# Performance work log

Hardware: AMD Instinct MI355X
Metric: run time of the kernel (lower is better)

Reference implementation:

```python
import jax, jax.numpy as jnp
import numpy as np

BLOCKS = (1, 2, 3, 4)      # (block_size, offset=0) from max_block_size=4
BLOCK_MULT = 12            # lcm(1,2,3,4)
DS = 4                     # downsample_factor
MAX_BS = 4                 # max block size (also pos_conv kernel size)
DIM = 512
VOCAB = 256


def _masked_mean(t, m, axis):
    # t: [..., L, D], m: [..., L] bool -> mean over axis with mask, 0 where empty
    mf = m[..., None].astype(t.dtype)
    num = jnp.sum(t * mf, axis=axis)
    tot = jnp.sum(mf, axis=axis)
    mean = num / jnp.clip(tot, 1.0)
    return jnp.where(tot == 0.0, jnp.zeros_like(mean), mean)


def setup_inputs() -> dict:
    key = jax.random.key(0)
    ks = jax.random.split(key, 8)
    B, S = 8, 2048
    return {
        "x": jax.random.randint(ks[0], (B, S), 0, VOCAB),
        "mask": jnp.ones((B, S), dtype=bool),
        "emb": jax.random.normal(ks[1], (VOCAB, DIM), jnp.float32) * 0.02,
        "dw_w": jax.random.normal(ks[2], (MAX_BS, 1, DIM), jnp.float32) * 0.1,   # depthwise kernel (W, I=1, O=DIM)
        "dw_b": jnp.zeros((DIM,), jnp.float32),
        "pw_w": jax.random.normal(ks[3], (1, DIM, DIM), jnp.float32) * 0.03,     # pointwise 1x1 conv
        "pw_b": jnp.zeros((DIM,), jnp.float32),
        "score_w": jax.random.normal(ks[4], (DIM, 1), jnp.float32) * 0.05,
        "score_b": jnp.zeros((1,), jnp.float32),
    }


def reference(x, mask, emb, dw_w, dw_b, pw_w, pw_b, score_w, score_b):
    B, S = x.shape
    D = DIM
    trunc = ((S + DS - 1) // DS) * DS  # next_divisible_length(S, DS); equals S here

    h = emb[x]                                              # [B,S,D]
    h = jnp.pad(h, ((0, 0), (0, MAX_BS - 1), (0, 0)))       # right pad for VALID conv
    dn = jax.lax.conv_dimension_numbers(h.shape, dw_w.shape, ('NWC', 'WIO', 'NWC'))
    h = jax.lax.conv_general_dilated(h, dw_w, (1,), 'VALID',
                                     dimension_numbers=dn,
                                     feature_group_count=D) + dw_b  # depthwise -> [B,S,D]
    h = jnp.einsum('bsd,de->bse', h, pw_w[0]) + pw_b                # pointwise

    # pad seq to multiple of lcm of block sizes
    Sp = ((h.shape[1] + BLOCK_MULT - 1) // BLOCK_MULT) * BLOCK_MULT
    pad = Sp - h.shape[1]
    h = jnp.pad(h, ((0, 0), (0, pad), (0, 0)))
    m = jnp.pad(mask.astype(bool), ((0, 0), (0, pad)), constant_values=False)

    reprs, rmasks = [], []
    for bsz in BLOCKS:  # fixed small set of block sizes (offset=0 for all)
        nb = Sp // bsz
        g = h.reshape(B, nb, bsz, D)
        mg = m.reshape(B, nb, bsz)
        r = _masked_mean(g, mg, axis=2)                       # [B,nb,D]
        reprs.append(jnp.repeat(r, bsz, axis=1))              # [B,Sp,D]
        rmasks.append(jnp.repeat(jnp.any(mg, axis=-1), bsz, axis=1))

    block_reprs = jnp.stack(reprs, axis=2)    # [B,Sp,M,D]
    block_masks = jnp.stack(rmasks, axis=2)   # [B,Sp,M]

    scores = (block_reprs @ score_w)[..., 0] + score_b[0]     # [B,Sp,M]
    max_neg = -jnp.finfo(scores.dtype).max
    scores = jnp.where(block_masks, scores, max_neg)
    scores = jnp.nan_to_num(jax.nn.softmax(scores, axis=2), nan=0.0)

    # consensus attention over positions
    sim = jnp.einsum('bim,bjm->bij', scores, scores)          # [B,Sp,Sp]
    cm = m[:, :, None] & m[:, None, :]
    sim = jnp.where(cm, sim, max_neg)
    attn = jnp.nan_to_num(jax.nn.softmax(sim, axis=-1), nan=0.0)
    scores = jnp.einsum('bij,bjm->bim', attn, scores)

    out = jnp.einsum('bsmd,bsm->bsd', block_reprs, scores)    # weighted combine
    out = out[:, :trunc]
    mt = m[:, :trunc]

    nl = trunc // DS
    xb = out.reshape(B, nl, DS, D)
    mb = mt.reshape(B, nl, DS)
    out = _masked_mean(xb, mb, axis=2)                        # [B, S/DS, D]
    out_mask = jnp.any(mb, axis=-1)
    return out, out_mask
```

## Files before the change

### kernel.cpp

```cpp
#include <hip/hip_runtime.h>
#include <stdint.h>
#include <stddef.h>

typedef __bf16 bf16_t;
typedef bf16_t bf16x4v __attribute__((ext_vector_type(4)));
typedef bf16_t bf16x8v __attribute__((ext_vector_type(8)));
typedef float  f32x4   __attribute__((ext_vector_type(4)));

#define NBATCH 8
#define SEQ    2048
#define DIM    512
#define SP     2052
#define NB2    1026
#define NB3    684
#define NB4    513
#define NL     512
#define NJC    8
#define JCH    257

static __device__ __forceinline__ f32x4 ldbf4(const bf16_t* p) {
  bf16x4v v = *(const bf16x4v*)p;
  f32x4 r;
  r.x = (float)v[0]; r.y = (float)v[1]; r.z = (float)v[2]; r.w = (float)v[3];
  return r;
}
static __device__ __forceinline__ void stbf4(bf16_t* p, f32x4 v) {
  bf16x4v o;
  o[0] = (bf16_t)v.x; o[1] = (bf16_t)v.y; o[2] = (bf16_t)v.z; o[3] = (bf16_t)v.w;
  *(bf16x4v*)p = o;
}

static __device__ __forceinline__ void gload_lds16(const void* g, void* l) {
  __builtin_amdgcn_global_load_lds(
      (const __attribute__((address_space(1))) void*)g,
      (__attribute__((address_space(3))) void*)l, 16, 0, 0);
}

#define GA_WT   256
#define GA_MASK 65
#define GA_A    (NBATCH * SEQ / 2)
__global__ __launch_bounds__(256) void kA_prep(
    const float* __restrict__ pw, bf16_t* __restrict__ Wt,
    const void* __restrict__ mraw, float* __restrict__ mask01,
    const int* __restrict__ x, const float* __restrict__ emb,
    const float* __restrict__ dww, const float* __restrict__ dwb,
    bf16_t* __restrict__ A) {
  const int bx = blockIdx.x, t = threadIdx.x;
  if (bx < GA_WT) {
    __shared__ float T[32][33];
    int ti = bx >> 4, tj = bx & 15;
    int r = t >> 3, c0 = (t & 7) * 4;
    f32x4 v = *(const f32x4*)(pw + (size_t)(ti * 32 + r) * DIM + tj * 32 + c0);
    T[c0 + 0][r] = v.x; T[c0 + 1][r] = v.y;
    T[c0 + 2][r] = v.z; T[c0 + 3][r] = v.w;
    __syncthreads();
    bf16x4v o;
    o[0] = (bf16_t)T[r][c0 + 0]; o[1] = (bf16_t)T[r][c0 + 1];
    o[2] = (bf16_t)T[r][c0 + 2]; o[3] = (bf16_t)T[r][c0 + 3];
    *(bf16x4v*)(Wt + (size_t)(tj * 32 + r) * DIM + ti * 32 + c0) = o;
    return;
  }
  if (bx < GA_WT + GA_MASK) {
    int idx = (bx - GA_WT) * 256 + t;
    if (idx >= NBATCH * SP) return;
    int b = idx / SP, s = idx - b * SP;
    const unsigned char* mb = (const unsigned char*)mraw;
    int u8 = 0;
#pragma unroll
    for (int i = 0; i < 64; i++)
      if ((i & 3) != 0 && mb[i] != 0) u8 = 1;
    float v = 0.f;
    if (s < SEQ) {
      int mi = b * SEQ + s;
      int nz = u8 ? (mb[mi] != 0) : (((const int*)mraw)[mi] != 0);
      v = nz ? 1.f : 0.f;
    }
    mask01[idx] = v;
    return;
  }
  int rp = bx - (GA_WT + GA_MASK);
  int row = rp * 2 + (t >> 7);
  int b = row >> 11, s = row & 2047;
  int d0 = (t & 127) * 4;
  f32x4 acc = *(const f32x4*)(dwb + d0);
#pragma unroll
  for (int tt = 0; tt < 4; tt++) {
    int sp = s + tt;
    if (sp < SEQ) {
      int v = x[b * SEQ + sp];
      f32x4 e = *(const f32x4*)(emb + (size_t)v * DIM + d0);
      f32x4 w = *(const f32x4*)(dww + tt * DIM + d0);
      acc += e * w;
    }
  }
  stbf4(A + (size_t)row * DIM + d0, acc);
}

#define BM 64
#define BN 128
#define BK 32
__global__ __launch_bounds__(256) void k2_gemm(
    const bf16_t* __restrict__ A, const bf16_t* __restrict__ Bt,
    const float* __restrict__ bias, bf16_t* __restrict__ H) {
  __shared__ __align__(16) bf16_t As[BM * BK];
  __shared__ __align__(16) bf16_t Bs[BN * BK];
  const int t = threadIdx.x;
  const int bid = blockIdx.x;
  const int xcd = bid & 7, loc = bid >> 3;
  const int mt = xcd * 32 + (loc >> 2);
  const int nt = loc & 3;
  const int m0 = mt * BM, n0 = nt * BN;
  const int lane = t & 63, wave = t >> 6;
  const int wm = (wave & 1) * 32, wn = (wave >> 1) * 64;
  const int mloc = lane & 15, quad = lane >> 4;

  f32x4 acc[2][4] = {};

  char* asd  = (char*)As + t * 16;
  char* bsd1 = (char*)Bs + t * 16;
  char* bsd2 = (char*)Bs + (t + 256) * 16;
  const int ar = t >> 2,           ak = (t & 3) * 8;
  const int br1 = t >> 2,          bk1 = (t & 3) * 8;
  const int br2 = (t + 256) >> 2,  bk2 = (t & 3) * 8;

  for (int k0 = 0; k0 < 512; k0 += BK) {
    gload_lds16(A + (size_t)(m0 + ar) * DIM + k0 + ak, asd);
    gload_lds16(Bt + (size_t)(n0 + br1) * DIM + k0 + bk1, bsd1);
    gload_lds16(Bt + (size_t)(n0 + br2) * DIM + k0 + bk2, bsd2);
    __syncthreads();
    bf16x8v af[2], bfr[4];
#pragma unroll
    for (int i = 0; i < 2; i++)
      af[i] = *(const bf16x8v*)&As[(wm + i * 16 + mloc) * BK + quad * 8];
#pragma unroll
    for (int i = 0; i < 4; i++)
      bfr[i] = *(const bf16x8v*)&Bs[(wn + i * 16 + mloc) * BK + quad * 8];
#pragma unroll
    for (int mi = 0; mi < 2; mi++)
#pragma unroll
      for (int ni = 0; ni < 4; ni++)
        acc[mi][ni] = __builtin_amdgcn_mfma_f32_16x16x32_bf16(
            af[mi], bfr[ni], acc[mi][ni], 0, 0, 0);
    __syncthreads();
  }
#pragma unroll
  for (int ni = 0; ni < 4; ni++) {
    int col = n0 + wn + ni * 16 + mloc;
    float bv = bias[col];
#pragma unroll
    for (int mi = 0; mi < 2; mi++) {
      int rbase = m0 + wm + mi * 16 + quad * 4;
#pragma unroll
      for (int r = 0; r < 4; r++)
        H[(size_t)(rbase + r) * DIM + col] = (bf16_t)(acc[mi][ni][r] + bv);
    }
  }
}

__global__ __launch_bounds__(128) void kB_levels(
    const bf16_t* __restrict__ H, const float* __restrict__ mask01,
    const float* __restrict__ sw, const float* __restrict__ sbp,
    bf16_t* __restrict__ R2, bf16_t* __restrict__ R3, bf16_t* __restrict__ R4,
    float* __restrict__ P) {
  const int b = blockIdx.x, c = blockIdx.y;
  const int s0 = c * 12;
  const int t = threadIdx.x;
  const int d0 = t * 4;
  const float sb = sbp[0];

  f32x4 h[12];
  float ms[12], p[12];
  f32x4 swv = *(const f32x4*)(sw + d0);
#pragma unroll
  for (int i = 0; i < 12; i++) {
    int s = s0 + i;
    ms[i] = mask01[b * SP + s];
    if (s < SEQ) {
      h[i] = ldbf4(H + ((size_t)b * SEQ + s) * DIM + d0);
    } else {
      h[i].x = h[i].y = h[i].z = h[i].w = 0.f;
    }
    p[i] = h[i].x * swv.x + h[i].y * swv.y + h[i].z * swv.z + h[i].w * swv.w;
  }
#pragma unroll
  for (int j = 0; j < 6; j++) {
    int i0 = 2 * j;
    float cc = ms[i0] + ms[i0 + 1];
    f32x4 sm = h[i0] * ms[i0] + h[i0 + 1] * ms[i0 + 1];
    float sc = cc > 0.f ? 1.f / cc : 0.f;
    stbf4(R2 + ((size_t)b * NB2 + (c * 6 + j)) * DIM + d0, sm * sc);
  }
#pragma unroll
  for (int j = 0; j < 4; j++) {
    int i0 = 3 * j;
    float cc = ms[i0] + ms[i0 + 1] + ms[i0 + 2];
    f32x4 sm = h[i0] * ms[i0] + h[i0 + 1] * ms[i0 + 1] + h[i0 + 2] * ms[i0 + 2];
    float sc = cc > 0.f ? 1.f / cc : 0.f;
    stbf4(R3 + ((size_t)b * NB3 + (c * 4 + j)) * DIM + d0, sm * sc);
  }
#pragma unroll
  for (int j = 0; j < 3; j++) {
    int i0 = 4 * j;
    float cc = ms[i0] + ms[i0 + 1] + ms[i0 + 2] + ms[i0 + 3];
    f32x4 sm = h[i0] * ms[i0] + h[i0 + 1] * ms[i0 + 1] +
               h[i0 + 2] * ms[i0 + 2] + h[i0 + 3] * ms[i0 + 3];
    float sc = cc > 0.f ? 1.f / cc : 0.f;
    stbf4(R4 + ((size_t)b * NB4 + (c * 3 + j)) * DIM + d0, sm * sc);
  }
#pragma unroll
  for (int off = 32; off > 0; off >>= 1)
#pragma unroll
    for (int i = 0; i < 12; i++) p[i] += __shfl_down(p[i], off);
  __shared__ float hsw[2][12];
  int lane = t & 63, wv = t >> 6;
  if (lane == 0)
#pragma unroll
    for (int i = 0; i < 12; i++) hsw[wv][i] = p[i];
  __syncthreads();
#define HSUM(i) (hsw[0][i] + hsw[1][i])
  if (t < 12) {
    int i = t;
    float m1 = ms[i];
    float v1 = HSUM(i) * m1 + sb;
    int i2 = i & ~1;
    float cc2 = ms[i2] + ms[i2 + 1];
    float s2 = HSUM(i2) * ms[i2] + HSUM(i2 + 1) * ms[i2 + 1];
    float v2 = (cc2 > 0.f ? s2 / cc2 : 0.f) + sb;
    int i3 = (i >= 9) ? 9 : (i >= 6) ? 6 : (i >= 3) ? 3 : 0;
    float cc3 = ms[i3] + ms[i3 + 1] + ms[i3 + 2];
    float s3 = HSUM(i3) * ms[i3] + HSUM(i3 + 1) * ms[i3 + 1] +
               HSUM(i3 + 2) * ms[i3 + 2];
    float v3 = (cc3 > 0.f ? s3 / cc3 : 0.f) + sb;
    int i4 = i & ~3;
    float cc4 = ms[i4] + ms[i4 + 1] + ms[i4 + 2] + ms[i4 + 3];
    float s4 = HSUM(i4) * ms[i4] + HSUM(i4 + 1) * ms[i4 + 1] +
               HSUM(i4 + 2) * ms[i4 + 2] + HSUM(i4 + 3) * ms[i4 + 3];
    float v4 = (cc4 > 0.f ? s4 / cc4 : 0.f) + sb;
    const float NEG = -3.0e38f;
    float a1 = m1 > 0.f ? v1 : NEG, a2 = cc2 > 0.f ? v2 : NEG;
    float a3 = cc3 > 0.f ? v3 : NEG, a4 = cc4 > 0.f ? v4 : NEG;
    float mx = fmaxf(fmaxf(a1, a2), fmaxf(a3, a4));
    f32x4 o;
    if (mx <= NEG) {
      o.x = o.y = o.z = o.w = 0.25f;
    } else {
      float e1 = m1 > 0.f ? __expf(v1 - mx) : 0.f;
      float e2 = cc2 > 0.f ? __expf(v2 - mx) : 0.f;
      float e3 = cc3 > 0.f ? __expf(v3 - mx) : 0.f;
      float e4 = cc4 > 0.f ? __expf(v4 - mx) : 0.f;
      float inv = 1.f / (e1 + e2 + e3 + e4);
      o.x = e1 * inv; o.y = e2 * inv; o.z = e3 * inv; o.w = e4 * inv;
    }
    *(f32x4*)(P + ((size_t)b * SP + s0 + i) * 4) = o;
  }
#undef HSUM
}

__global__ __launch_bounds__(128) void k5_attn(
    const float* __restrict__ P, const float* __restrict__ mask01,
    float* __restrict__ Wacc) {
  const int b = blockIdx.x, it = blockIdx.y, jc = blockIdx.z;
  const int t = threadIdx.x;
  __shared__ f32x4 Q[JCH];
  __shared__ float c2w[2];
  const int j0 = jc * JCH;
  const int len = (j0 + JCH <= SP) ? JCH : (SP - j0);
  float cnt0 = 0.f;
  for (int j = t; j < len; j += 128) {
    f32x4 q = *(const f32x4*)(P + ((size_t)b * SP + j0 + j) * 4);
    float mf = mask01[b * SP + j0 + j];
    if (mf == 0.f) {
      q.x = q.y = q.z = q.w = 0.f;
      cnt0 += 1.f;
    }
    Q[j] = q;
  }
#pragma unroll
  for (int off = 32; off > 0; off >>= 1) cnt0 += __shfl_down(cnt0, off);
  if ((t & 63) == 0) c2w[t >> 6] = cnt0;
  __syncthreads();
  const float nmask = c2w[0] + c2w[1];
  const int i = it * 128 + t;
  f32x4 qi = *(const f32x4*)(P + ((size_t)b * SP + i) * 4);
  float den = -nmask;
  f32x4 acc; acc.x = acc.y = acc.z = acc.w = 0.f;
  for (int j = 0; j < len; j++) {
    f32x4 pj = Q[j];
    float sim = qi.x * pj.x + qi.y * pj.y + qi.z * pj.z + qi.w * pj.w;
    float e = __expf(sim);
    den += e;
    acc += e * pj;
  }
  float* wp = Wacc + (((size_t)jc * NBATCH + b) * SEQ + i) * 5;
  wp[0] = acc.x; wp[1] = acc.y; wp[2] = acc.z; wp[3] = acc.w; wp[4] = den;
}

__global__ __launch_bounds__(128) void k6_out(
    const bf16_t* __restrict__ H, const bf16_t* __restrict__ R2,
    const bf16_t* __restrict__ R3, const bf16_t* __restrict__ R4,
    const float* __restrict__ mask01, const float* __restrict__ Wacc,
    float* __restrict__ out, float* __restrict__ omask) {
  const int b = blockIdx.x, l = blockIdx.y;
  const int t = threadIdx.x;
  const int d0 = t * 4;
  __shared__ f32x4 wsh[4];
  __shared__ float msh[4];
  if (t < 32) {
    int si = t >> 3, jc = t & 7;
    int s = l * 4 + si;
    const float* wp = Wacc + (((size_t)jc * NBATCH + b) * SEQ + s) * 5;
    float n0 = wp[0], n1 = wp[1], n2 = wp[2], n3 = wp[3], dn = wp[4];
#pragma unroll
    for (int off = 4; off > 0; off >>= 1) {
      n0 += __shfl_down(n0, off); n1 += __shfl_down(n1, off);
      n2 += __shfl_down(n2, off); n3 += __shfl_down(n3, off);
      dn += __shfl_down(dn, off);
    }
    if ((t & 7) == 0) {
      float inv = dn > 0.f ? 1.f / dn : 0.f;
      f32x4 w; w.x = n0 * inv; w.y = n1 * inv; w.z = n2 * inv; w.w = n3 * inv;
      wsh[si] = w;
      msh[si] = mask01[b * SP + s];
    }
  }
  __syncthreads();
  f32x4 o; o.x = o.y = o.z = o.w = 0.f;
  float cnt = 0.f;
#pragma unroll
  for (int si = 0; si < 4; si++) {
    int s = l * 4 + si;
    float m = msh[si];
    f32x4 w = wsh[si];
    f32x4 r1 = ldbf4(H + ((size_t)b * SEQ + s) * DIM + d0);
    f32x4 r2 = ldbf4(R2 + ((size_t)b * NB2 + (s >> 1)) * DIM + d0);
    f32x4 r3 = ldbf4(R3 + ((size_t)b * NB3 + (s / 3)) * DIM + d0);
    f32x4 r4 = ldbf4(R4 + ((size_t)b * NB4 + (s >> 2)) * DIM + d0);
    o += m * (w.x * r1 + w.y * r2 + w.z * r3 + w.w * r4);
    cnt += m;
  }
  float inv = cnt > 0.f ? 1.f / cnt : 0.f;
  o *= inv;
  *(f32x4*)(out + ((size_t)b * NL + l) * DIM + d0) = o;
  if (t == 0) omask[b * NL + l] = cnt > 0.f ? 1.f : 0.f;
}

extern "C" void kernel_launch(void* const* d_in, const int* in_sizes, int n_in,
                              void* d_out, int out_size, void* d_ws, size_t ws_size,
                              hipStream_t stream) {
  const int*   x    = (const int*)d_in[0];
  const void*  mraw = d_in[1];
  const float* emb  = (const float*)d_in[2];
  const float* dww  = (const float*)d_in[3];
  const float* dwb  = (const float*)d_in[4];
  const float* pw   = (const float*)d_in[5];
  const float* pwb  = (const float*)d_in[6];
  const float* sw   = (const float*)d_in[7];
  const float* sb   = (const float*)d_in[8];

  char* ws = (char*)d_ws;
  size_t off = 0;
  auto alloc = [&](size_t bytes) {
    size_t o = off;
    off = (off + bytes + 255) & ~(size_t)255;
    return o;
  };
  bf16_t* A    = (bf16_t*)(ws + alloc((size_t)NBATCH * SEQ * DIM * 2));
  bf16_t* H    = (bf16_t*)(ws + alloc((size_t)NBATCH * SEQ * DIM * 2));
  bf16_t* Wt   = (bf16_t*)(ws + alloc((size_t)DIM * DIM * 2));
  bf16_t* R2   = (bf16_t*)(ws + alloc((size_t)NBATCH * NB2 * DIM * 2));
  bf16_t* R3   = (bf16_t*)(ws + alloc((size_t)NBATCH * NB3 * DIM * 2));
  bf16_t* R4   = (bf16_t*)(ws + alloc((size_t)NBATCH * NB4 * DIM * 2));
  float* mask01 = (float*)(ws + alloc((size_t)NBATCH * SP * 4));
  float* P     = (float*)(ws + alloc((size_t)NBATCH * SP * 4 * 4));
  float* Wacc  = (float*)(ws + alloc((size_t)NJC * NBATCH * SEQ * 5 * 4));

  float* out   = (float*)d_out;
  float* omask = out + (size_t)NBATCH * NL * DIM;

  kA_prep<<<GA_WT + GA_MASK + GA_A, 256, 0, stream>>>(pw, Wt, mraw, mask01,
                                                      x, emb, dww, dwb, A);
  k2_gemm<<<1024, 256, 0, stream>>>(A, Wt, pwb, H);
  kB_levels<<<dim3(NBATCH, 171), 128, 0, stream>>>(H, mask01, sw, sb,
                                                   R2, R3, R4, P);
  k5_attn<<<dim3(NBATCH, 16, NJC), 128, 0, stream>>>(P, mask01, Wacc);
  k6_out<<<dim3(NBATCH, NL), 128, 0, stream>>>(H, R2, R3, R4, mask01, Wacc,
                                               out, omask);
}
```

Baseline: 141.0 us.

## Fuse consensus attention with output combine and recompute block means on the fly

The R2/R3/R4 block-mean tensors are no longer materialized. They are recomputed from H inside the output kernel. The attention kernel and the output kernel are merged into one kernel that loads all of P into shared memory, reduces over the full sequence across 16 lanes per row, and then does the weighted combine and downsample mean, which removes the Wacc round trip and one launch. In exchange, each block redundantly recomputes the full attention reduction for only 16 rows and reads a halo of H rows.

```diff
diff --git a/kernel.cpp b/kernel.cpp
--- a/kernel.cpp
+++ b/kernel.cpp
@@ -11,12 +11,7 @@
 #define SEQ    2048
 #define DIM    512
 #define SP     2052
-#define NB2    1026
-#define NB3    684
-#define NB4    513
 #define NL     512
-#define NJC    8
-#define JCH    257
 
 static __device__ __forceinline__ f32x4 ldbf4(const bf16_t* p) {
   bf16x4v v = *(const bf16x4v*)p;
@@ -157,10 +152,9 @@
   }
 }
 
-__global__ __launch_bounds__(128) void kB_levels(
+__global__ __launch_bounds__(128) void kB_p(
     const bf16_t* __restrict__ H, const float* __restrict__ mask01,
     const float* __restrict__ sw, const float* __restrict__ sbp,
-    bf16_t* __restrict__ R2, bf16_t* __restrict__ R3, bf16_t* __restrict__ R4,
     float* __restrict__ P) {
   const int b = blockIdx.x, c = blockIdx.y;
   const int s0 = c * 12;
@@ -168,7 +162,6 @@
   const int d0 = t * 4;
   const float sb = sbp[0];
 
-  f32x4 h[12];
   float ms[12], p[12];
   f32x4 swv = *(const f32x4*)(sw + d0);
 #pragma unroll
@@ -176,36 +169,11 @@
     int s = s0 + i;
     ms[i] = mask01[b * SP + s];
     if (s < SEQ) {
-      h[i] = ldbf4(H + ((size_t)b * SEQ + s) * DIM + d0);
+      f32x4 h = ldbf4(H + ((size_t)b * SEQ + s) * DIM + d0);
+      p[i] = h.x * swv.x + h.y * swv.y + h.z * swv.z + h.w * swv.w;
     } else {
-      h[i].x = h[i].y = h[i].z = h[i].w = 0.f;
-    }
-    p[i] = h[i].x * swv.x + h[i].y * swv.y + h[i].z * swv.z + h[i].w * swv.w;
-  }
-#pragma unroll
-  for (int j = 0; j < 6; j++) {
-    int i0 = 2 * j;
-    float cc = ms[i0] + ms[i0 + 1];
-    f32x4 sm = h[i0] * ms[i0] + h[i0 + 1] * ms[i0 + 1];
-    float sc = cc > 0.f ? 1.f / cc : 0.f;
-    stbf4(R2 + ((size_t)b * NB2 + (c * 6 + j)) * DIM + d0, sm * sc);
-  }
-#pragma unroll
-  for (int j = 0; j < 4; j++) {
-    int i0 = 3 * j;
-    float cc = ms[i0] + ms[i0 + 1] + ms[i0 + 2];
-    f32x4 sm = h[i0] * ms[i0] + h[i0 + 1] * ms[i0 + 1] + h[i0 + 2] * ms[i0 + 2];
-    float sc = cc > 0.f ? 1.f / cc : 0.f;
-    stbf4(R3 + ((size_t)b * NB3 + (c * 4 + j)) * DIM + d0, sm * sc);
-  }
-#pragma unroll
-  for (int j = 0; j < 3; j++) {
-    int i0 = 4 * j;
-    float cc = ms[i0] + ms[i0 + 1] + ms[i0 + 2] + ms[i0 + 3];
-    f32x4 sm = h[i0] * ms[i0] + h[i0 + 1] * ms[i0 + 1] +
-               h[i0 + 2] * ms[i0 + 2] + h[i0 + 3] * ms[i0 + 3];
-    float sc = cc > 0.f ? 1.f / cc : 0.f;
-    stbf4(R4 + ((size_t)b * NB4 + (c * 3 + j)) * DIM + d0, sm * sc);
+      p[i] = 0.f;
+    }
   }
 #pragma unroll
   for (int off = 32; off > 0; off >>= 1)
@@ -256,92 +224,123 @@
 #undef HSUM
 }
 
-__global__ __launch_bounds__(128) void k5_attn(
-    const float* __restrict__ P, const float* __restrict__ mask01,
-    float* __restrict__ Wacc) {
-  const int b = blockIdx.x, it = blockIdx.y, jc = blockIdx.z;
+#define KS  16
+#define KJL 129
+__global__ __launch_bounds__(256) void k56_out(
+    const bf16_t* __restrict__ H, const float* __restrict__ P,
+    const float* __restrict__ mask01, float* __restrict__ out,
+    float* __restrict__ omask) {
+  const int b = blockIdx.x, yb = blockIdx.y;
   const int t = threadIdx.x;
-  __shared__ f32x4 Q[JCH];
-  __shared__ float c2w[2];
-  const int j0 = jc * JCH;
-  const int len = (j0 + JCH <= SP) ? JCH : (SP - j0);
+  const int S0 = yb * KS;
+  __shared__ f32x4 Q[SP];
+  __shared__ f32x4 wsh[KS];
+  __shared__ float msh[KS + 8];
+  __shared__ float red[4];
+
   float cnt0 = 0.f;
-  for (int j = t; j < len; j += 128) {
-    f32x4 q = *(const f32x4*)(P + ((size_t)b * SP + j0 + j) * 4);
-    float mf = mask01[b * SP + j0 + j];
-    if (mf == 0.f) {
+  for (int j = t; j < SP; j += 256) {
+    f32x4 q = *(const f32x4*)(P + ((size_t)b * SP + j) * 4);
+    if (mask01[b * SP + j] == 0.f) {
       q.x = q.y = q.z = q.w = 0.f;
       cnt0 += 1.f;
     }
     Q[j] = q;
   }
+  if (t < KS + 8) {
+    int s = S0 - 2 + t;
+    msh[t] = (s >= 0 && s < SP) ? mask01[b * SP + s] : 0.f;
+  }
 #pragma unroll
   for (int off = 32; off > 0; off >>= 1) cnt0 += __shfl_down(cnt0, off);
-  if ((t & 63) == 0) c2w[t >> 6] = cnt0;
+  if ((t & 63) == 0) red[t >> 6] = cnt0;
   __syncthreads();
-  const float nmask = c2w[0] + c2w[1];
-  const int i = it * 128 + t;
-  f32x4 qi = *(const f32x4*)(P + ((size_t)b * SP + i) * 4);
-  float den = -nmask;
-  f32x4 acc; acc.x = acc.y = acc.z = acc.w = 0.f;
-  for (int j = 0; j < len; j++) {
-    f32x4 pj = Q[j];
-    float sim = qi.x * pj.x + qi.y * pj.y + qi.z * pj.z + qi.w * pj.w;
-    float e = __expf(sim);
-    den += e;
-    acc += e * pj;
-  }
-  float* wp = Wacc + (((size_t)jc * NBATCH + b) * SEQ + i) * 5;
-  wp[0] = acc.x; wp[1] = acc.y; wp[2] = acc.z; wp[3] = acc.w; wp[4] = den;
-}
-
-__global__ __launch_bounds__(128) void k6_out(
-    const bf16_t* __restrict__ H, const bf16_t* __restrict__ R2,
-    const bf16_t* __restrict__ R3, const bf16_t* __restrict__ R4,
-    const float* __restrict__ mask01, const float* __restrict__ Wacc,
-    float* __restrict__ out, float* __restrict__ omask) {
-  const int b = blockIdx.x, l = blockIdx.y;
-  const int t = threadIdx.x;
-  const int d0 = t * 4;
-  __shared__ f32x4 wsh[4];
-  __shared__ float msh[4];
-  if (t < 32) {
-    int si = t >> 3, jc = t & 7;
-    int s = l * 4 + si;
-    const float* wp = Wacc + (((size_t)jc * NBATCH + b) * SEQ + s) * 5;
-    float n0 = wp[0], n1 = wp[1], n2 = wp[2], n3 = wp[3], dn = wp[4];
-#pragma unroll
-    for (int off = 4; off > 0; off >>= 1) {
-      n0 += __shfl_down(n0, off); n1 += __shfl_down(n1, off);
-      n2 += __shfl_down(n2, off); n3 += __shfl_down(n3, off);
-      dn += __shfl_down(dn, off);
-    }
-    if ((t & 7) == 0) {
-      float inv = dn > 0.f ? 1.f / dn : 0.f;
-      f32x4 w; w.x = n0 * inv; w.y = n1 * inv; w.z = n2 * inv; w.w = n3 * inv;
-      wsh[si] = w;
-      msh[si] = mask01[b * SP + s];
+  const float nmask = red[0] + red[1] + red[2] + red[3];
+
+  {
+    const int il = t >> 4, jc = t & 15;
+    const f32x4 qi = Q[S0 + il];
+    int j0 = jc * KJL, j1 = j0 + KJL;
+    if (j1 > SP) j1 = SP;
+    f32x4 acc; acc.x = acc.y = acc.z = acc.w = 0.f;
+    float den = 0.f;
+    for (int j = j0; j < j1; j++) {
+      f32x4 pj = Q[j];
+      float sim = qi.x * pj.x + qi.y * pj.y + qi.z * pj.z + qi.w * pj.w;
+      float e = __expf(sim);
+      den += e;
+      acc += e * pj;
+    }
+#pragma unroll
+    for (int off = 8; off > 0; off >>= 1) {
+      acc.x += __shfl_down(acc.x, off); acc.y += __shfl_down(acc.y, off);
+      acc.z += __shfl_down(acc.z, off); acc.w += __shfl_down(acc.w, off);
+      den += __shfl_down(den, off);
+    }
+    if (jc == 0) {
+      den -= nmask;
+      float inv = den > 0.f ? 1.f / den : 0.f;
+      f32x4 w;
+      w.x = acc.x * inv; w.y = acc.y * inv;
+      w.z = acc.z * inv; w.w = acc.w * inv;
+      wsh[il] = w;
     }
   }
   __syncthreads();
-  f32x4 o; o.x = o.y = o.z = o.w = 0.f;
-  float cnt = 0.f;
-#pragma unroll
-  for (int si = 0; si < 4; si++) {
-    int s = l * 4 + si;
-    float m = msh[si];
-    f32x4 w = wsh[si];
-    f32x4 r1 = ldbf4(H + ((size_t)b * SEQ + s) * DIM + d0);
-    f32x4 r2 = ldbf4(R2 + ((size_t)b * NB2 + (s >> 1)) * DIM + d0);
-    f32x4 r3 = ldbf4(R3 + ((size_t)b * NB3 + (s / 3)) * DIM + d0);
-    f32x4 r4 = ldbf4(R4 + ((size_t)b * NB4 + (s >> 2)) * DIM + d0);
-    o += m * (w.x * r1 + w.y * r2 + w.z * r3 + w.w * r4);
-    cnt += m;
-  }
-  float inv = cnt > 0.f ? 1.f / cnt : 0.f;
-  o *= inv;
-  *(f32x4*)(out + ((size_t)b * NL + l) * DIM + d0) = o;
-  if (t == 0) omask[b * NL + l] = cnt > 0.f ? 1.f : 0.f;
+
+#pragma unroll
+  for (int it = 0; it < 2; it++) {
+    const int slot = it * 256 + t;
+    const int ll = slot >> 7;
+    const int d0 = (slot & 127) * 4;
+    const int sb = ll * 4;
+    f32x4 h[8]; float mk[8];
+#pragma unroll
+    for (int k = 0; k < 8; k++) {
+      mk[k] = msh[sb + k];
+      int sg = S0 + sb - 2 + k;
+      sg = sg < 0 ? 0 : (sg > SEQ - 1 ? SEQ - 1 : sg);
+      h[k] = ldbf4(H + ((size_t)b * SEQ + sg) * DIM + d0);
+    }
+    float c4 = mk[2] + mk[3] + mk[4] + mk[5];
+    float i4 = c4 > 0.f ? 1.f / c4 : 0.f;
+    f32x4 r4 = (h[2] * mk[2] + h[3] * mk[3] + h[4] * mk[4] + h[5] * mk[5]) * i4;
+    float c2a = mk[2] + mk[3], c2b = mk[4] + mk[5];
+    f32x4 r2a = (h[2] * mk[2] + h[3] * mk[3]) * (c2a > 0.f ? 1.f / c2a : 0.f);
+    f32x4 r2b = (h[4] * mk[4] + h[5] * mk[5]) * (c2b > 0.f ? 1.f / c2b : 0.f);
+    const f32x4 w0 = wsh[sb], w1 = wsh[sb + 1];
+    const f32x4 w2 = wsh[sb + 2], w3 = wsh[sb + 3];
+#define MEAN3(K)                                                         \
+    ((h[K] * mk[K] + h[(K) + 1] * mk[(K) + 1] + h[(K) + 2] * mk[(K) + 2]) * \
+     ((mk[K] + mk[(K) + 1] + mk[(K) + 2]) > 0.f                          \
+          ? 1.f / (mk[K] + mk[(K) + 1] + mk[(K) + 2]) : 0.f))
+    f32x4 o;
+    const int r = (S0 + sb) % 3;
+    if (r == 0) {
+      f32x4 A = MEAN3(2), B = MEAN3(5);
+      o = mk[2] * (w0.x * h[2] + w0.y * r2a + w0.z * A + w0.w * r4)
+        + mk[3] * (w1.x * h[3] + w1.y * r2a + w1.z * A + w1.w * r4)
+        + mk[4] * (w2.x * h[4] + w2.y * r2b + w2.z * A + w2.w * r4)
+        + mk[5] * (w3.x * h[5] + w3.y * r2b + w3.z * B + w3.w * r4);
+    } else if (r == 1) {
+      f32x4 A = MEAN3(1), B = MEAN3(4);
+      o = mk[2] * (w0.x * h[2] + w0.y * r2a + w0.z * A + w0.w * r4)
+        + mk[3] * (w1.x * h[3] + w1.y * r2a + w1.z * A + w1.w * r4)
+        + mk[4] * (w2.x * h[4] + w2.y * r2b + w2.z * B + w2.w * r4)
+        + mk[5] * (w3.x * h[5] + w3.y * r2b + w3.z * B + w3.w * r4);
+    } else {
+      f32x4 A = MEAN3(0), B = MEAN3(3);
+      o = mk[2] * (w0.x * h[2] + w0.y * r2a + w0.z * A + w0.w * r4)
+        + mk[3] * (w1.x * h[3] + w1.y * r2a + w1.z * B + w1.w * r4)
+        + mk[4] * (w2.x * h[4] + w2.y * r2b + w2.z * B + w2.w * r4)
+        + mk[5] * (w3.x * h[5] + w3.y * r2b + w3.z * B + w3.w * r4);
+    }
+#undef MEAN3
+    o *= i4;
+    const int l = yb * 4 + ll;
+    *(f32x4*)(out + ((size_t)b * NL + l) * DIM + d0) = o;
+    if (d0 == 0) omask[b * NL + l] = c4 > 0.f ? 1.f : 0.f;
+  }
 }
 
 extern "C" void kernel_launch(void* const* d_in, const int* in_sizes, int n_in,
@@ -364,15 +363,11 @@
     off = (off + bytes + 255) & ~(size_t)255;
     return o;
   };
-  bf16_t* A    = (bf16_t*)(ws + alloc((size_t)NBATCH * SEQ * DIM * 2));
-  bf16_t* H    = (bf16_t*)(ws + alloc((size_t)NBATCH * SEQ * DIM * 2));
-  bf16_t* Wt   = (bf16_t*)(ws + alloc((size_t)DIM * DIM * 2));
-  bf16_t* R2   = (bf16_t*)(ws + alloc((size_t)NBATCH * NB2 * DIM * 2));
-  bf16_t* R3   = (bf16_t*)(ws + alloc((size_t)NBATCH * NB3 * DIM * 2));
-  bf16_t* R4   = (bf16_t*)(ws + alloc((size_t)NBATCH * NB4 * DIM * 2));
+  bf16_t* A     = (bf16_t*)(ws + alloc((size_t)NBATCH * SEQ * DIM * 2));
+  bf16_t* H     = (bf16_t*)(ws + alloc((size_t)NBATCH * SEQ * DIM * 2));
+  bf16_t* Wt    = (bf16_t*)(ws + alloc((size_t)DIM * DIM * 2));
   float* mask01 = (float*)(ws + alloc((size_t)NBATCH * SP * 4));
-  float* P     = (float*)(ws + alloc((size_t)NBATCH * SP * 4 * 4));
-  float* Wacc  = (float*)(ws + alloc((size_t)NJC * NBATCH * SEQ * 5 * 4));
+  float* P      = (float*)(ws + alloc((size_t)NBATCH * SP * 4 * 4));
 
   float* out   = (float*)d_out;
   float* omask = out + (size_t)NBATCH * NL * DIM;
@@ -380,9 +375,6 @@
   kA_prep<<<GA_WT + GA_MASK + GA_A, 256, 0, stream>>>(pw, Wt, mraw, mask01,
                                                       x, emb, dww, dwb, A);
   k2_gemm<<<1024, 256, 0, stream>>>(A, Wt, pwb, H);
-  kB_levels<<<dim3(NBATCH, 171), 128, 0, stream>>>(H, mask01, sw, sb,
-                                                   R2, R3, R4, P);
-  k5_attn<<<dim3(NBATCH, 16, NJC), 128, 0, stream>>>(P, mask01, Wacc);
-  k6_out<<<dim3(NBATCH, NL), 128, 0, stream>>>(H, R2, R3, R4, mask01, Wacc,
-                                               out, omask);
-}
+  kB_p<<<dim3(NBATCH, 171), 128, 0, stream>>>(H, mask01, sw, sb, P);
+  k56_out<<<dim3(NBATCH, 128), 256, 0, stream>>>(H, P, mask01, out, omask);
+}
```

Result: slower. 143.9 us (+2.1%).
